# Performance work log

Measured on AMD Instinct MI355X. Metric: run time of the kernel, lower is better.

## Reference

```python
import jax, jax.numpy as jnp
import numpy as np

B, N, T, D, H = 64, 207, 24, 128, 8
DK = D // H
EPS = 1e-5


def setup_inputs() -> dict:
    key = jax.random.key(0)
    ks = jax.random.split(key, 18)
    s = 1.0 / np.sqrt(D)
    inp = {
        "hidden": jax.random.normal(ks[0], (B, N, T, D), jnp.float32),
        "matrix": jax.random.uniform(ks[1], (B, T, N, N), jnp.float32) / N,
        "Wq": jax.random.normal(ks[2], (D, D), jnp.float32) * s,
        "bq": jnp.zeros((D,), jnp.float32),
        "Wk": jax.random.normal(ks[3], (D, D), jnp.float32) * s,
        "bk": jnp.zeros((D,), jnp.float32),
        "Wv": jax.random.normal(ks[4], (D, D), jnp.float32) * s,
        "bv": jnp.zeros((D,), jnp.float32),
        "Wo": jax.random.normal(ks[5], (D, D), jnp.float32) * s,
        "bo": jnp.zeros((D,), jnp.float32),
        "Wgcn": jax.random.normal(ks[6], (D, D), jnp.float32) * s,
        "bgcn": jnp.zeros((D,), jnp.float32),
        "Wgate": jax.random.normal(ks[7], (D, 2 * D), jnp.float32) * (1.0 / np.sqrt(2 * D)),
        "bgate": jnp.zeros((D,), jnp.float32),
        "gamma": jnp.ones((D,), jnp.float32),
        "beta": jnp.zeros((D,), jnp.float32),
    }
    return inp


def reference(hidden, matrix, Wq, bq, Wk, bk, Wv, bv, Wo, bo,
              Wgcn, bgcn, Wgate, bgate, gamma, beta):
    # ---- GCN branch: per-timestep A·X then channel mixing (dmodel->dmodel)
    # hidden: [B,N,T,D], matrix: [B,T,N,N] -> aggregated [B,N,T,D]
    agg = jnp.einsum('bntc,btnm->bmtc', hidden, matrix)
    gcn_out = agg @ Wgcn.T + bgcn                       # [B,N,T,D]

    # ---- Causal multi-head temporal attention
    q = (hidden @ Wq.T + bq).reshape(B, N, T, H, DK)
    k = (hidden @ Wk.T + bk).reshape(B, N, T, H, DK)
    v = (hidden @ Wv.T + bv).reshape(B, N, T, H, DK)
    scale = 1.0 / np.sqrt(DK)
    scores = jnp.einsum('bnthe,bnshe->bnhts', q, k)     # [B,N,H,T,T]
    causal = jnp.triu(jnp.ones((T, T), bool), k=1)      # mask future
    scores = jnp.where(causal, -jnp.inf, scores)
    attn = jax.nn.softmax(scale * scores, axis=-1)
    ctx = jnp.einsum('bnhts,bnshd->bnthd', attn, v).reshape(B, N, T, D)
    attn_out = ctx @ Wo.T + bo                          # [B,N,T,D]

    # ---- Gated fusion: concat -> linear -> batchnorm (training stats) -> sigmoid
    gate_in = jnp.concatenate([gcn_out, attn_out], axis=-1)  # [B,N,T,2D]
    g = gate_in @ Wgate.T + bgate                            # [B,N,T,D]
    mean = jnp.mean(g, axis=(0, 1, 2))
    var = jnp.var(g, axis=(0, 1, 2))
    g = (g - mean) * jax.lax.rsqrt(var + EPS) * gamma + beta
    z = jax.nn.sigmoid(g)
    return z * gcn_out + (1.0 - z) * attn_out
```

## Files before the change

kernel.cpp:

```cpp
#include <hip/hip_runtime.h>

#define B_ 64
#define N_ 207
#define T_ 24
#define D_ 128
#define H_ 8
#define MROWS (B_*N_*T_)
#define SELEMS ((size_t)MROWS * D_)
#define NBLK_FB 768
#define BNROWS_FB 414
#define NBLK_FUSED (MROWS/128)
#define EPS_ 1e-5f

typedef __attribute__((ext_vector_type(8))) short s16x8;
typedef __attribute__((ext_vector_type(4))) float f32x4;

#define MFMA16(a,b,c) __builtin_amdgcn_mfma_f32_16x16x32_bf16(a,b,c,0,0,0)

__device__ __forceinline__ float bfu2f(unsigned short u) {
  return __uint_as_float(((unsigned int)u) << 16);
}
__device__ __forceinline__ unsigned short f2bfu(float f) {
  unsigned int x = __float_as_uint(f);
  return (unsigned short)((x + 0x7fffu + ((x >> 16) & 1u)) >> 16);
}
__device__ __forceinline__ unsigned int packbf2(float lo, float hi) {
  return (unsigned int)f2bfu(lo) | ((unsigned int)f2bfu(hi) << 16);
}

__global__ __launch_bounds__(256) void k_wcast(
    const float* __restrict__ Wq, const float* __restrict__ Wk,
    const float* __restrict__ Wv, const float* __restrict__ Wo,
    const float* __restrict__ Wgcn, const float* __restrict__ Wgate,
    unsigned short* __restrict__ out)
{
  const int idx4 = (blockIdx.x * 256 + threadIdx.x) * 4;
  if (idx4 >= 114688) return;
  const float* src; int off;
  if      (idx4 < 16384) { src = Wq;    off = idx4; }
  else if (idx4 < 32768) { src = Wk;    off = idx4 - 16384; }
  else if (idx4 < 49152) { src = Wv;    off = idx4 - 32768; }
  else if (idx4 < 65536) { src = Wo;    off = idx4 - 49152; }
  else if (idx4 < 81920) { src = Wgcn;  off = idx4 - 65536; }
  else                   { src = Wgate; off = idx4 - 81920; }
  const float4 v = *(const float4*)(src + off);
  ushort4 u;
  u.x = f2bfu(v.x); u.y = f2bfu(v.y); u.z = f2bfu(v.z); u.w = f2bfu(v.w);
  *(ushort4*)(out + idx4) = u;
}

__device__ __forceinline__ void gcn_load(
    const float* __restrict__ mbase, const float* __restrict__ hbase,
    int m0, int nn, int cb, int ch,
    float va[8], float vb[8], float ha[8], float hb[8])
{
  const int n_r0 = ch*32 + nn, n_r1 = n_r0 + 1;
  const bool rv0 = (n_r0 < N_), rv1 = (n_r1 < N_);
  const size_t nc0 = (size_t)(rv0 ? n_r0 : 0);
  const size_t nc1 = (size_t)(rv1 ? n_r1 : 0);
  {
    const float* r0 = mbase + nc0*N_ + m0 + cb;
    const float* r1 = mbase + nc1*N_ + m0 + cb;
    #pragma unroll
    for (int j = 0; j < 2; ++j) {
      const int mg = m0 + cb + j*4;
      if (mg + 3 < N_) {
        const float4 x0 = *(const float4*)(r0 + j*4);
        const float4 x1 = *(const float4*)(r1 + j*4);
        va[j*4+0]=x0.x; va[j*4+1]=x0.y; va[j*4+2]=x0.z; va[j*4+3]=x0.w;
        vb[j*4+0]=x1.x; vb[j*4+1]=x1.y; vb[j*4+2]=x1.z; vb[j*4+3]=x1.w;
      } else {
        #pragma unroll
        for (int e = 0; e < 4; ++e) {
          const bool ok = (mg + e) < N_;
          va[j*4+e] = ok ? r0[j*4+e] : 0.f;
          vb[j*4+e] = ok ? r1[j*4+e] : 0.f;
        }
      }
    }
    #pragma unroll
    for (int e = 0; e < 8; ++e) {
      if (!rv0) va[e] = 0.f;
      if (!rv1) vb[e] = 0.f;
    }
  }
  {
    const float* r0 = hbase + nc0*(T_*D_) + cb;
    const float* r1 = hbase + nc1*(T_*D_) + cb;
    const float4 x0a = *(const float4*)(r0);
    const float4 x0b = *(const float4*)(r0 + 4);
    const float4 x1a = *(const float4*)(r1);
    const float4 x1b = *(const float4*)(r1 + 4);
    ha[0]=x0a.x; ha[1]=x0a.y; ha[2]=x0a.z; ha[3]=x0a.w;
    ha[4]=x0b.x; ha[5]=x0b.y; ha[6]=x0b.z; ha[7]=x0b.w;
    hb[0]=x1a.x; hb[1]=x1a.y; hb[2]=x1a.z; hb[3]=x1a.w;
    hb[4]=x1b.x; hb[5]=x1b.y; hb[6]=x1b.z; hb[7]=x1b.w;
    #pragma unroll
    for (int e = 0; e < 8; ++e) {
      if (!rv0) ha[e] = 0.f;
      if (!rv1) hb[e] = 0.f;
    }
  }
}

__global__ __launch_bounds__(256) void k_gcn2(
    const float* __restrict__ hidden, const float* __restrict__ matrix,
    const unsigned short* __restrict__ Wgcnb, const float* __restrict__ bgcn,
    unsigned short* __restrict__ gcn)
{
  __shared__ __align__(16) unsigned char smem[40960];
  unsigned short* GsAll = (unsigned short*)smem;

  const int tid = threadIdx.x;
  const int w = tid >> 6, l = tid & 63;
  const int lr = l & 15, lg = l >> 4;
  const int m0 = blockIdx.x * 128;
  const int by = (int)blockIdx.y;
  const int b = by / T_, t = by % T_;

  const int nn = (tid & 15) * 2;
  const int cb = (tid >> 4) * 8;

  const float* mbase = matrix + (size_t)(b*T_ + t)*N_*N_;
  const float* hbase = hidden + (size_t)b*N_*T_*D_ + (size_t)t*D_;

  f32x4 acc1[2][8];
  #pragma unroll
  for (int mt = 0; mt < 2; mt++)
    #pragma unroll
    for (int nt = 0; nt < 8; nt++)
      #pragma unroll
      for (int e = 0; e < 4; e++) acc1[mt][nt][e] = 0.f;

  float va[8], vb[8], ha[8], hb[8];
  gcn_load(mbase, hbase, m0, nn, cb, 0, va, vb, ha, hb);

  #pragma unroll
  for (int ch = 0; ch < 7; ++ch) {
    unsigned char* base = smem + ((ch & 1) ? 20480 : 0);
    unsigned int* M32 = (unsigned int*)base;
    unsigned int* H32 = (unsigned int*)(base + 10240);
    #pragma unroll
    for (int e = 0; e < 8; ++e)
      M32[(cb + e)*20 + (tid & 15)] = packbf2(va[e], vb[e]);
    #pragma unroll
    for (int e = 0; e < 8; ++e)
      H32[(cb + e)*20 + (tid & 15)] = packbf2(ha[e], hb[e]);
    if (ch < 6)
      gcn_load(mbase, hbase, m0, nn, cb, ch + 1, va, vb, ha, hb);
    __syncthreads();
    const unsigned short* M16 = (const unsigned short*)M32;
    const unsigned short* H16 = (const unsigned short*)H32;
    const s16x8 af0 = *(const s16x8*)(M16 + (size_t)(w*32 +  0 + lr)*40 + lg*8);
    const s16x8 af1 = *(const s16x8*)(M16 + (size_t)(w*32 + 16 + lr)*40 + lg*8);
    #pragma unroll
    for (int nt = 0; nt < 8; ++nt) {
      const s16x8 bf = *(const s16x8*)(H16 + (size_t)(nt*16 + lr)*40 + lg*8);
      acc1[0][nt] = MFMA16(af0, bf, acc1[0][nt]);
      acc1[1][nt] = MFMA16(af1, bf, acc1[1][nt]);
    }
  }

  __syncthreads();
  unsigned short* gs = GsAll + (size_t)w * (32*136);
  #pragma unroll
  for (int nt = 0; nt < 8; nt++)
    #pragma unroll
    for (int mt = 0; mt < 2; mt++)
      #pragma unroll
      for (int r = 0; r < 4; r++)
        gs[(mt*16 + lg*4 + r)*136 + nt*16 + lr] = f2bfu(acc1[mt][nt][r]);

  f32x4 acc2[2][8];
  #pragma unroll
  for (int mt = 0; mt < 2; mt++)
    #pragma unroll
    for (int nt = 0; nt < 8; nt++)
      #pragma unroll
      for (int e = 0; e < 4; e++) acc2[mt][nt][e] = 0.f;

  #pragma unroll
  for (int ks = 0; ks < 4; ++ks) {
    const s16x8 a0 = *(const s16x8*)(gs + (size_t)( 0 + lr)*136 + ks*32 + lg*8);
    const s16x8 a1 = *(const s16x8*)(gs + (size_t)(16 + lr)*136 + ks*32 + lg*8);
    #pragma unroll
    for (int nt = 0; nt < 8; ++nt) {
      const s16x8 bf = *(const s16x8*)(Wgcnb + (size_t)(nt*16 + lr)*D_ + ks*32 + lg*8);
      acc2[0][nt] = MFMA16(a0, bf, acc2[0][nt]);
      acc2[1][nt] = MFMA16(a1, bf, acc2[1][nt]);
    }
  }

  #pragma unroll
  for (int nt = 0; nt < 8; nt++) {
    const float bsc = bgcn[nt*16 + lr];
    #pragma unroll
    for (int mt = 0; mt < 2; mt++)
      #pragma unroll
      for (int r = 0; r < 4; r++)
        gs[(mt*16 + lg*4 + r)*136 + nt*16 + lr] = f2bfu(acc2[mt][nt][r] + bsc);
  }
  const size_t Obase = ((size_t)b*N_ + (m0 + w*32))*(size_t)(T_*D_) + (size_t)t*D_;
  #pragma unroll
  for (int p = 0; p < 8; p++) {
    const int c = p*64 + l;
    const int row = c >> 4, c8 = (c & 15) * 8;
    const int gm = m0 + w*32 + row;
    if (gm < N_) {
      const s16x8 v = *(const s16x8*)(gs + row*136 + c8);
      *(s16x8*)(gcn + Obase + (size_t)row*(T_*D_) + c8) = v;
    }
  }
}

__global__ __launch_bounds__(256) void k_attn3(
    const float* __restrict__ hidden,
    const unsigned short* __restrict__ Wqb, const unsigned short* __restrict__ Wkb,
    const unsigned short* __restrict__ Wvb, const unsigned short* __restrict__ Wob,
    const float* __restrict__ bq, const float* __restrict__ bk,
    const float* __restrict__ bv, const float* __restrict__ bo,
    unsigned short* __restrict__ attnO)
{
  __shared__ __align__(16) unsigned short Xs[32*136];
  __shared__ __align__(16) unsigned short Qs[32*136];
  __shared__ __align__(16) unsigned short Ks[32*136];
  __shared__ __align__(16) unsigned short Vt[128*40];
  __shared__ __align__(16) unsigned short Ps[4][32*40];
  const int tid = threadIdx.x;
  const int w = tid >> 6, l = tid & 63;
  const int lr = l & 15, lg = l >> 4;
  const size_t bn = blockIdx.x;
  const float* X = hidden + bn * (size_t)(T_*D_);

  for (int i = tid; i < 32*16; i += 256) {
    const int row = i >> 4, g8 = (i & 15) * 8;
    s16x8 v;
    if (row < T_) {
      const float4 a  = *(const float4*)(X + (size_t)row*D_ + g8);
      const float4 b2 = *(const float4*)(X + (size_t)row*D_ + g8 + 4);
      v[0]=(short)f2bfu(a.x);  v[1]=(short)f2bfu(a.y);
      v[2]=(short)f2bfu(a.z);  v[3]=(short)f2bfu(a.w);
      v[4]=(short)f2bfu(b2.x); v[5]=(short)f2bfu(b2.y);
      v[6]=(short)f2bfu(b2.z); v[7]=(short)f2bfu(b2.w);
    } else {
      #pragma unroll
      for (int e = 0; e < 8; e++) v[e] = 0;
    }
    *(s16x8*)&Xs[row*136 + g8] = v;
  }
  __syncthreads();

  s16x8 af[2][4];
  #pragma unroll
  for (int mt = 0; mt < 2; mt++)
    #pragma unroll
    for (int ks = 0; ks < 4; ks++)
      af[mt][ks] = *(const s16x8*)&Xs[(mt*16 + lr)*136 + ks*32 + lg*8];
  __syncthreads();

  const unsigned short* Wp[3] = {Wqb, Wkb, Wvb};
  const float*          bp[3] = {bq, bk, bv};
  #pragma unroll
  for (int o = 0; o < 3; o++) {
    f32x4 acc[2][2];
    #pragma unroll
    for (int mt = 0; mt < 2; mt++)
      #pragma unroll
      for (int nt = 0; nt < 2; nt++)
        #pragma unroll
        for (int e = 0; e < 4; e++) acc[mt][nt][e] = 0.f;
    #pragma unroll
    for (int ks = 0; ks < 4; ks++) {
      #pragma unroll
      for (int nt = 0; nt < 2; nt++) {
        const s16x8 bf = *(const s16x8*)(Wp[o] + (size_t)(w*32 + nt*16 + lr)*D_ + ks*32 + lg*8);
        acc[0][nt] = MFMA16(af[0][ks], bf, acc[0][nt]);
        acc[1][nt] = MFMA16(af[1][ks], bf, acc[1][nt]);
      }
    }
    #pragma unroll
    for (int nt = 0; nt < 2; nt++) {
      const float bb = bp[o][w*32 + nt*16 + lr];
      #pragma unroll
      for (int mt = 0; mt < 2; mt++)
        #pragma unroll
        for (int r = 0; r < 4; r++) {
          const unsigned short hv = f2bfu(acc[mt][nt][r] + bb);
          const int trow = mt*16 + lg*4 + r;
          const int dcol = w*32 + nt*16 + lr;
          if (o == 0)      Qs[trow*136 + dcol] = hv;
          else if (o == 1) Ks[trow*136 + dcol] = hv;
          else             Vt[dcol*40 + trow] = hv;
        }
    }
  }

  unsigned short* Pw = Ps[w];
  #pragma unroll
  for (int hi = 0; hi < 2; hi++) {
    const int hh = 2*w + hi;
    s16x8 zv;
    #pragma unroll
    for (int e = 0; e < 8; e++) zv[e] = 0;
    s16x8 aq[2], bkf[2];
    #pragma unroll
    for (int mt = 0; mt < 2; mt++) {
      s16x8 tv = zv;
      if (lg < 2) tv = *(const s16x8*)&Qs[(mt*16 + lr)*136 + hh*16 + lg*8];
      aq[mt] = tv;
    }
    #pragma unroll
    for (int nt = 0; nt < 2; nt++) {
      s16x8 tv = zv;
      if (lg < 2) tv = *(const s16x8*)&Ks[(nt*16 + lr)*136 + hh*16 + lg*8];
      bkf[nt] = tv;
    }
    f32x4 accS[2][2];
    #pragma unroll
    for (int mt = 0; mt < 2; mt++)
      #pragma unroll
      for (int nt = 0; nt < 2; nt++) {
        f32x4 z4; z4[0]=0.f; z4[1]=0.f; z4[2]=0.f; z4[3]=0.f;
        accS[mt][nt] = MFMA16(aq[mt], bkf[nt], z4);
      }
    #pragma unroll
    for (int mt = 0; mt < 2; mt++) {
      #pragma unroll
      for (int r = 0; r < 4; r++) {
        const int t = mt*16 + lg*4 + r;
        const bool m0 = (lr <= t), m1 = (16 + lr <= t);
        float e0 = m0 ? __expf(0.25f * accS[mt][0][r]) : 0.f;
        float e1 = m1 ? __expf(0.25f * accS[mt][1][r]) : 0.f;
        float den = e0 + e1;
        den += __shfl_xor(den, 1);
        den += __shfl_xor(den, 2);
        den += __shfl_xor(den, 4);
        den += __shfl_xor(den, 8);
        const float rd = 1.f / den;
        Pw[t*40 + lr]      = f2bfu(e0 * rd);
        Pw[t*40 + 16 + lr] = f2bfu(e1 * rd);
      }
    }
    s16x8 ap[2];
    #pragma unroll
    for (int mt = 0; mt < 2; mt++)
      ap[mt] = *(const s16x8*)&Pw[(mt*16 + lr)*40 + lg*8];
    const s16x8 bvf = *(const s16x8*)&Vt[(hh*16 + lr)*40 + lg*8];
    f32x4 accP[2];
    #pragma unroll
    for (int mt = 0; mt < 2; mt++) {
      f32x4 z4; z4[0]=0.f; z4[1]=0.f; z4[2]=0.f; z4[3]=0.f;
      accP[mt] = MFMA16(ap[mt], bvf, z4);
    }
    #pragma unroll
    for (int mt = 0; mt < 2; mt++)
      #pragma unroll
      for (int r = 0; r < 4; r++) {
        const int t = mt*16 + lg*4 + r;
        if (t < T_) Xs[t*136 + hh*16 + lr] = f2bfu(accP[mt][r]);
      }
  }
  __syncthreads();

  s16x8 cf[2][4];
  #pragma unroll
  for (int mt = 0; mt < 2; mt++)
    #pragma unroll
    for (int ks = 0; ks < 4; ks++)
      cf[mt][ks] = *(const s16x8*)&Xs[(mt*16 + lr)*136 + ks*32 + lg*8];
  f32x4 acc2[2][2];
  #pragma unroll
  for (int mt = 0; mt < 2; mt++)
    #pragma unroll
    for (int nt = 0; nt < 2; nt++)
      #pragma unroll
      for (int e = 0; e < 4; e++) acc2[mt][nt][e] = 0.f;
  #pragma unroll
  for (int ks = 0; ks < 4; ks++) {
    #pragma unroll
    for (int nt = 0; nt < 2; nt++) {
      const s16x8 bf = *(const s16x8*)(Wob + (size_t)(w*32 + nt*16 + lr)*D_ + ks*32 + lg*8);
      acc2[0][nt] = MFMA16(cf[0][ks], bf, acc2[0][nt]);
      acc2[1][nt] = MFMA16(cf[1][ks], bf, acc2[1][nt]);
    }
  }
  #pragma unroll
  for (int nt = 0; nt < 2; nt++) {
    const float bb = bo[w*32 + nt*16 + lr];
    #pragma unroll
    for (int mt = 0; mt < 2; mt++)
      #pragma unroll
      for (int r = 0; r < 4; r++)
        Qs[(mt*16 + lg*4 + r)*136 + w*32 + nt*16 + lr] =
            f2bfu(acc2[mt][nt][r] + bb);
  }
  __syncthreads();
  unsigned short* O = attnO + bn * (size_t)(T_*D_);
  for (int i = tid; i < 24*16; i += 256) {
    const int row = i >> 4, g8 = (i & 15) * 8;
    *(s16x8*)(O + (size_t)row*D_ + g8) = *(const s16x8*)&Qs[row*136 + g8];
  }
}

template<bool STATS>
__global__ __launch_bounds__(256) void k_gate(
    const unsigned short* __restrict__ A0, const unsigned short* __restrict__ A1,
    const unsigned short* __restrict__ Wb, const float* __restrict__ bias,
    float* __restrict__ Out, float* __restrict__ psum, float* __restrict__ psq)
{
  __shared__ float lbs[4*128], lbq[4*128];
  const int tid = threadIdx.x;
  const int w = tid >> 6, l = tid & 63;
  const int lr = l & 15, lg = l >> 4;
  const size_t m0 = (size_t)blockIdx.x * 128 + w * 32;

  f32x4 acc[2][8];
  #pragma unroll
  for (int mt = 0; mt < 2; mt++)
    #pragma unroll
    for (int nt = 0; nt < 8; nt++)
      #pragma unroll
      for (int e = 0; e < 4; e++) acc[mt][nt][e] = 0.f;

  #pragma unroll
  for (int ks = 0; ks < 8; ks++) {
    const unsigned short* Asrc = (ks >= 4) ? A1 : A0;
    const int kk = (ks >= 4) ? ks - 4 : ks;
    const s16x8 a0 = *(const s16x8*)(Asrc + (m0 +  0 + lr)*D_ + kk*32 + lg*8);
    const s16x8 a1 = *(const s16x8*)(Asrc + (m0 + 16 + lr)*D_ + kk*32 + lg*8);
    #pragma unroll
    for (int nt = 0; nt < 8; nt++) {
      const s16x8 bf = *(const s16x8*)(Wb + (size_t)(nt*16 + lr)*256 + ks*32 + lg*8);
      acc[0][nt] = MFMA16(a0, bf, acc[0][nt]);
      acc[1][nt] = MFMA16(a1, bf, acc[1][nt]);
    }
  }

  #pragma unroll
  for (int nt = 0; nt < 8; nt++) {
    const float b = bias[nt*16 + lr];
    float s = 0.f, q = 0.f;
    #pragma unroll
    for (int mt = 0; mt < 2; mt++)
      #pragma unroll
      for (int r = 0; r < 4; r++) {
        const float v = acc[mt][nt][r] + b;
        Out[(m0 + mt*16 + lg*4 + r)*D_ + nt*16 + lr] = v;
        if (STATS) { s += v; q += v*v; }
      }
    if (STATS) {
      s += __shfl_xor(s, 16); s += __shfl_xor(s, 32);
      q += __shfl_xor(q, 16); q += __shfl_xor(q, 32);
      if (lg == 0) {
        lbs[w*128 + nt*16 + lr] = s;
        lbq[w*128 + nt*16 + lr] = q;
      }
    }
  }
  if (STATS) {
    __syncthreads();
    if (tid < 128) {
      const float ss = lbs[tid] + lbs[128 + tid] + lbs[256 + tid] + lbs[384 + tid];
      const float qq = lbq[tid] + lbq[128 + tid] + lbq[256 + tid] + lbq[384 + tid];
      psum[(size_t)blockIdx.x*128 + tid] = ss;
      psq [(size_t)blockIdx.x*128 + tid] = qq;
    }
  }
}

__global__ __launch_bounds__(256) void k_bnstats(
    const float* __restrict__ g, float* __restrict__ psum, float* __restrict__ psq)
{
  const int tid = threadIdx.x;
  const int c4 = (tid & 31) * 4, sub = tid >> 5;
  const size_t r0 = (size_t)blockIdx.x * BNROWS_FB;
  float4 s = make_float4(0.f,0.f,0.f,0.f), q = make_float4(0.f,0.f,0.f,0.f);
  for (int i = sub; i < BNROWS_FB; i += 8) {
    const float4 x = *(const float4*)(g + (r0 + i)*D_ + c4);
    s.x += x.x; s.y += x.y; s.z += x.z; s.w += x.w;
    q.x += x.x*x.x; q.y += x.y*x.y; q.z += x.z*x.z; q.w += x.w*x.w;
  }
  __shared__ float ls[8*128], lq[8*128];
  *(float4*)&ls[sub*128 + c4] = s;
  *(float4*)&lq[sub*128 + c4] = q;
  __syncthreads();
  if (tid < 128) {
    float ss = 0.f, qq = 0.f;
    #pragma unroll
    for (int k = 0; k < 8; k++) { ss += ls[k*128 + tid]; qq += lq[k*128 + tid]; }
    psum[(size_t)blockIdx.x*128 + tid] = ss;
    psq [(size_t)blockIdx.x*128 + tid] = qq;
  }
}

__global__ __launch_bounds__(1024) void k_bnfinal(
    const float* __restrict__ psum, const float* __restrict__ psq, int nblk,
    float* __restrict__ meanv, float* __restrict__ invstdv)
{
  const int tid = threadIdx.x;
  const int sub = tid >> 7, ch = tid & 127;
  float s = 0.f, q = 0.f;
  for (int i = sub; i < nblk; i += 8) {
    s += psum[(size_t)i*128 + ch];
    q += psq [(size_t)i*128 + ch];
  }
  __shared__ float ls[8*128], lq[8*128];
  ls[sub*128 + ch] = s; lq[sub*128 + ch] = q;
  __syncthreads();
  if (tid < 128) {
    float ss = 0.f, qq = 0.f;
    #pragma unroll
    for (int k = 0; k < 8; k++) { ss += ls[k*128 + tid]; qq += lq[k*128 + tid]; }
    const float mean = ss / (float)MROWS;
    const float var  = qq / (float)MROWS - mean*mean;
    meanv[tid] = mean;
    invstdv[tid] = rsqrtf(var + EPS_);
  }
}

__global__ __launch_bounds__(256) void k_final(
    float* __restrict__ g,
    const unsigned short* __restrict__ gcn, const unsigned short* __restrict__ attn,
    const float* __restrict__ meanv, const float* __restrict__ invstdv,
    const float* __restrict__ gamma, const float* __restrict__ beta)
{
  const size_t tot4 = SELEMS >> 2;
  for (size_t i4 = (size_t)blockIdx.x*blockDim.x + threadIdx.x; i4 < tot4;
       i4 += (size_t)gridDim.x*blockDim.x) {
    const int c4 = (int)(i4 & 31) * 4;
    const float4 gv = ((const float4*)g)[i4];
    const ushort4 gc = ((const ushort4*)gcn)[i4];
    const ushort4 at = ((const ushort4*)attn)[i4];
    const float4 m4 = *(const float4*)(meanv + c4);
    const float4 s4 = *(const float4*)(invstdv + c4);
    const float4 ga = *(const float4*)(gamma + c4);
    const float4 be = *(const float4*)(beta + c4);
    float4 outv;
    { const float y = (gv.x - m4.x)*s4.x*ga.x + be.x;
      const float z = 1.f/(1.f + __expf(-y));
      outv.x = z*bfu2f(gc.x) + (1.f - z)*bfu2f(at.x); }
    { const float y = (gv.y - m4.y)*s4.y*ga.y + be.y;
      const float z = 1.f/(1.f + __expf(-y));
      outv.y = z*bfu2f(gc.y) + (1.f - z)*bfu2f(at.y); }
    { const float y = (gv.z - m4.z)*s4.z*ga.z + be.z;
      const float z = 1.f/(1.f + __expf(-y));
      outv.z = z*bfu2f(gc.z) + (1.f - z)*bfu2f(at.z); }
    { const float y = (gv.w - m4.w)*s4.w*ga.w + be.w;
      const float z = 1.f/(1.f + __expf(-y));
      outv.w = z*bfu2f(gc.w) + (1.f - z)*bfu2f(at.w); }
    ((float4*)g)[i4] = outv;
  }
}

extern "C" void kernel_launch(void* const* d_in, const int* in_sizes, int n_in,
                              void* d_out, int out_size, void* d_ws, size_t ws_size,
                              hipStream_t stream)
{
  (void)in_sizes; (void)n_in; (void)out_size;
  const float* hidden = (const float*)d_in[0];
  const float* matrix = (const float*)d_in[1];
  const float* Wq   = (const float*)d_in[2];  const float* bq    = (const float*)d_in[3];
  const float* Wk   = (const float*)d_in[4];  const float* bk    = (const float*)d_in[5];
  const float* Wv   = (const float*)d_in[6];  const float* bv    = (const float*)d_in[7];
  const float* Wo   = (const float*)d_in[8];  const float* bo    = (const float*)d_in[9];
  const float* Wgcn = (const float*)d_in[10]; const float* bgcn  = (const float*)d_in[11];
  const float* Wgate= (const float*)d_in[12]; const float* bgate = (const float*)d_in[13];
  const float* gamma= (const float*)d_in[14]; const float* beta  = (const float*)d_in[15];
  float* out = (float*)d_out;

  unsigned short* WB = (unsigned short*)d_ws;
  unsigned short* Wqb    = WB;
  unsigned short* Wkb    = WB + 16384;
  unsigned short* Wvb    = WB + 32768;
  unsigned short* Wob    = WB + 49152;
  unsigned short* Wgcnb  = WB + 65536;
  unsigned short* Wgateb = WB + 81920;
  unsigned short* X1     = WB + 114688;
  unsigned short* X2     = X1 + SELEMS;
  float* psum    = (float*)(X2 + SELEMS);

  const size_t base_bytes = (size_t)(WB + 114688 - (unsigned short*)d_ws)*2
                          + 2*SELEMS*2;
  const size_t fused_bytes = base_bytes + ((size_t)NBLK_FUSED*128*2 + 256)*4;
  const bool fused = (ws_size >= fused_bytes);
  const int nblk = fused ? NBLK_FUSED : NBLK_FB;
  float* psq     = psum + (size_t)nblk*128;
  float* meanv   = psq  + (size_t)nblk*128;
  float* invstdv = meanv + 128;

  k_wcast<<<112, 256, 0, stream>>>(Wq, Wk, Wv, Wo, Wgcn, Wgate, WB);
  k_gcn2 <<<dim3(2, B_*T_), 256, 0, stream>>>(hidden, matrix, Wgcnb, bgcn, X2);
  k_attn3<<<B_*N_, 256, 0, stream>>>(hidden, Wqb, Wkb, Wvb, Wob,
                                     bq, bk, bv, bo, X1);
  if (fused) {
    k_gate<true><<<MROWS/128, 256, 0, stream>>>(X2, X1, Wgateb, bgate, out, psum, psq);
  } else {
    k_gate<false><<<MROWS/128, 256, 0, stream>>>(X2, X1, Wgateb, bgate, out, psum, psq);
    k_bnstats<<<NBLK_FB, 256, 0, stream>>>(out, psum, psq);
  }
  k_bnfinal<<<1, 1024, 0, stream>>>(psum, psq, nblk, meanv, invstdv);
  k_final<<<2048, 256, 0, stream>>>(out, X2, X1, meanv, invstdv, gamma, beta);
}
```

Measured before the change: 750.9 us.

## Recompute gate GEMM in final pass instead of storing fp32 gate tensor

```diff
diff --git a/kernel.cpp b/kernel.cpp
--- a/kernel.cpp
+++ b/kernel.cpp
@@ -1,4 +1,5 @@
 #include <hip/hip_runtime.h>
+#include <hip/hip_bf16.h>
 
 #define B_ 64
 #define N_ 207
@@ -21,8 +22,9 @@
   return __uint_as_float(((unsigned int)u) << 16);
 }
 __device__ __forceinline__ unsigned short f2bfu(float f) {
-  unsigned int x = __float_as_uint(f);
-  return (unsigned short)((x + 0x7fffu + ((x >> 16) & 1u)) >> 16);
+  union { __hip_bfloat16 h; unsigned short u; } cv;
+  cv.h = __float2bfloat16(f);
+  return cv.u;
 }
 __device__ __forceinline__ unsigned int packbf2(float lo, float hi) {
   return (unsigned int)f2bfu(lo) | ((unsigned int)f2bfu(hi) << 16);
@@ -234,19 +236,16 @@
 
   for (int i = tid; i < 32*16; i += 256) {
     const int row = i >> 4, g8 = (i & 15) * 8;
-    s16x8 v;
     if (row < T_) {
       const float4 a  = *(const float4*)(X + (size_t)row*D_ + g8);
       const float4 b2 = *(const float4*)(X + (size_t)row*D_ + g8 + 4);
-      v[0]=(short)f2bfu(a.x);  v[1]=(short)f2bfu(a.y);
-      v[2]=(short)f2bfu(a.z);  v[3]=(short)f2bfu(a.w);
-      v[4]=(short)f2bfu(b2.x); v[5]=(short)f2bfu(b2.y);
-      v[6]=(short)f2bfu(b2.z); v[7]=(short)f2bfu(b2.w);
+      uint4 u;
+      u.x = packbf2(a.x, a.y);   u.y = packbf2(a.z, a.w);
+      u.z = packbf2(b2.x, b2.y); u.w = packbf2(b2.z, b2.w);
+      *(uint4*)&Xs[row*136 + g8] = u;
     } else {
-      #pragma unroll
-      for (int e = 0; e < 8; e++) v[e] = 0;
-    }
-    *(s16x8*)&Xs[row*136 + g8] = v;
+      *(uint4*)&Xs[row*136 + g8] = make_uint4(0,0,0,0);
+    }
   }
   __syncthreads();
 
@@ -296,12 +295,12 @@
   }
 
   unsigned short* Pw = Ps[w];
+  s16x8 zv;
+  #pragma unroll
+  for (int e = 0; e < 8; e++) zv[e] = 0;
   #pragma unroll
   for (int hi = 0; hi < 2; hi++) {
     const int hh = 2*w + hi;
-    s16x8 zv;
-    #pragma unroll
-    for (int e = 0; e < 8; e++) zv[e] = 0;
     s16x8 aq[2], bkf[2];
     #pragma unroll
     for (int mt = 0; mt < 2; mt++) {
@@ -402,7 +401,7 @@
   }
 }
 
-template<bool STATS>
+template<bool WRITEG, bool STATS>
 __global__ __launch_bounds__(256) void k_gate(
     const unsigned short* __restrict__ A0, const unsigned short* __restrict__ A1,
     const unsigned short* __restrict__ Wb, const float* __restrict__ bias,
@@ -445,7 +444,7 @@
       #pragma unroll
       for (int r = 0; r < 4; r++) {
         const float v = acc[mt][nt][r] + b;
-        Out[(m0 + mt*16 + lg*4 + r)*D_ + nt*16 + lr] = v;
+        if (WRITEG) Out[(m0 + mt*16 + lg*4 + r)*D_ + nt*16 + lr] = v;
         if (STATS) { s += v; q += v*v; }
       }
     if (STATS) {
@@ -468,6 +467,77 @@
   }
 }
 
+__global__ __launch_bounds__(256) void k_final2(
+    const unsigned short* __restrict__ A0, const unsigned short* __restrict__ A1,
+    const unsigned short* __restrict__ Wb, const float* __restrict__ bias,
+    const float* __restrict__ scalev, const float* __restrict__ shiftv,
+    float* __restrict__ Out)
+{
+  __shared__ __align__(16) unsigned short lb[4][32*136];
+  const int tid = threadIdx.x;
+  const int w = tid >> 6, l = tid & 63;
+  const int lr = l & 15, lg = l >> 4;
+  const size_t m0 = (size_t)blockIdx.x * 128 + w * 32;
+
+  f32x4 acc[2][8];
+  #pragma unroll
+  for (int mt = 0; mt < 2; mt++)
+    #pragma unroll
+    for (int nt = 0; nt < 8; nt++)
+      #pragma unroll
+      for (int e = 0; e < 4; e++) acc[mt][nt][e] = 0.f;
+
+  #pragma unroll
+  for (int ks = 0; ks < 8; ks++) {
+    const unsigned short* Asrc = (ks >= 4) ? A1 : A0;
+    const int kk = (ks >= 4) ? ks - 4 : ks;
+    const s16x8 a0 = *(const s16x8*)(Asrc + (m0 +  0 + lr)*D_ + kk*32 + lg*8);
+    const s16x8 a1 = *(const s16x8*)(Asrc + (m0 + 16 + lr)*D_ + kk*32 + lg*8);
+    #pragma unroll
+    for (int nt = 0; nt < 8; nt++) {
+      const s16x8 bf = *(const s16x8*)(Wb + (size_t)(nt*16 + lr)*256 + ks*32 + lg*8);
+      acc[0][nt] = MFMA16(a0, bf, acc[0][nt]);
+      acc[1][nt] = MFMA16(a1, bf, acc[1][nt]);
+    }
+  }
+
+  #pragma unroll
+  for (int nt = 0; nt < 8; nt++) {
+    const float b = bias[nt*16 + lr];
+    #pragma unroll
+    for (int mt = 0; mt < 2; mt++)
+      #pragma unroll
+      for (int r = 0; r < 4; r++)
+        lb[w][(mt*16 + lg*4 + r)*136 + nt*16 + lr] = f2bfu(acc[mt][nt][r] + b);
+  }
+  #pragma unroll
+  for (int p = 0; p < 8; p++) {
+    const int c = p*64 + l;
+    const int row = c >> 4, c8 = (c & 15) * 8;
+    const size_t grow = m0 + row;
+    const s16x8 g8  = *(const s16x8*)&lb[w][row*136 + c8];
+    const s16x8 gc8 = *(const s16x8*)(A0 + grow*D_ + c8);
+    const s16x8 at8 = *(const s16x8*)(A1 + grow*D_ + c8);
+    const float4 sc0 = *(const float4*)(scalev + c8);
+    const float4 sc1 = *(const float4*)(scalev + c8 + 4);
+    const float4 sh0 = *(const float4*)(shiftv + c8);
+    const float4 sh1 = *(const float4*)(shiftv + c8 + 4);
+    const float scv[8] = {sc0.x,sc0.y,sc0.z,sc0.w,sc1.x,sc1.y,sc1.z,sc1.w};
+    const float shv[8] = {sh0.x,sh0.y,sh0.z,sh0.w,sh1.x,sh1.y,sh1.z,sh1.w};
+    float o[8];
+    #pragma unroll
+    for (int e = 0; e < 8; e++) {
+      const float y = bfu2f((unsigned short)g8[e]) * scv[e] + shv[e];
+      const float z = 1.f / (1.f + __expf(-y));
+      o[e] = z * bfu2f((unsigned short)gc8[e])
+           + (1.f - z) * bfu2f((unsigned short)at8[e]);
+    }
+    float* orow = Out + grow*D_ + c8;
+    *(float4*)orow       = make_float4(o[0], o[1], o[2], o[3]);
+    *(float4*)(orow + 4) = make_float4(o[4], o[5], o[6], o[7]);
+  }
+}
+
 __global__ __launch_bounds__(256) void k_bnstats(
     const float* __restrict__ g, float* __restrict__ psum, float* __restrict__ psq)
 {
@@ -495,7 +565,8 @@
 
 __global__ __launch_bounds__(1024) void k_bnfinal(
     const float* __restrict__ psum, const float* __restrict__ psq, int nblk,
-    float* __restrict__ meanv, float* __restrict__ invstdv)
+    const float* __restrict__ gamma, const float* __restrict__ beta,
+    float* __restrict__ scalev, float* __restrict__ shiftv)
 {
   const int tid = threadIdx.x;
   const int sub = tid >> 7, ch = tid & 127;
@@ -513,16 +584,17 @@
     for (int k = 0; k < 8; k++) { ss += ls[k*128 + tid]; qq += lq[k*128 + tid]; }
     const float mean = ss / (float)MROWS;
     const float var  = qq / (float)MROWS - mean*mean;
-    meanv[tid] = mean;
-    invstdv[tid] = rsqrtf(var + EPS_);
+    const float istd = rsqrtf(var + EPS_);
+    const float sc = istd * gamma[tid];
+    scalev[tid] = sc;
+    shiftv[tid] = beta[tid] - mean * sc;
   }
 }
 
 __global__ __launch_bounds__(256) void k_final(
     float* __restrict__ g,
     const unsigned short* __restrict__ gcn, const unsigned short* __restrict__ attn,
-    const float* __restrict__ meanv, const float* __restrict__ invstdv,
-    const float* __restrict__ gamma, const float* __restrict__ beta)
+    const float* __restrict__ scalev, const float* __restrict__ shiftv)
 {
   const size_t tot4 = SELEMS >> 2;
   for (size_t i4 = (size_t)blockIdx.x*blockDim.x + threadIdx.x; i4 < tot4;
@@ -531,21 +603,19 @@
     const float4 gv = ((const float4*)g)[i4];
     const ushort4 gc = ((const ushort4*)gcn)[i4];
     const ushort4 at = ((const ushort4*)attn)[i4];
-    const float4 m4 = *(const float4*)(meanv + c4);
-    const float4 s4 = *(const float4*)(invstdv + c4);
-    const float4 ga = *(const float4*)(gamma + c4);
-    const float4 be = *(const float4*)(beta + c4);
+    const float4 sc = *(const float4*)(scalev + c4);
+    const float4 sh = *(const float4*)(shiftv + c4);
     float4 outv;
-    { const float y = (gv.x - m4.x)*s4.x*ga.x + be.x;
+    { const float y = gv.x*sc.x + sh.x;
       const float z = 1.f/(1.f + __expf(-y));
       outv.x = z*bfu2f(gc.x) + (1.f - z)*bfu2f(at.x); }
-    { const float y = (gv.y - m4.y)*s4.y*ga.y + be.y;
+    { const float y = gv.y*sc.y + sh.y;
       const float z = 1.f/(1.f + __expf(-y));
       outv.y = z*bfu2f(gc.y) + (1.f - z)*bfu2f(at.y); }
-    { const float y = (gv.z - m4.z)*s4.z*ga.z + be.z;
+    { const float y = gv.z*sc.z + sh.z;
       const float z = 1.f/(1.f + __expf(-y));
       outv.z = z*bfu2f(gc.z) + (1.f - z)*bfu2f(at.z); }
-    { const float y = (gv.w - m4.w)*s4.w*ga.w + be.w;
+    { const float y = gv.w*sc.w + sh.w;
       const float z = 1.f/(1.f + __expf(-y));
       outv.w = z*bfu2f(gc.w) + (1.f - z)*bfu2f(at.w); }
     ((float4*)g)[i4] = outv;
@@ -585,19 +655,24 @@
   const bool fused = (ws_size >= fused_bytes);
   const int nblk = fused ? NBLK_FUSED : NBLK_FB;
   float* psq     = psum + (size_t)nblk*128;
-  float* meanv   = psq  + (size_t)nblk*128;
-  float* invstdv = meanv + 128;
+  float* scalev  = psq  + (size_t)nblk*128;
+  float* shiftv  = scalev + 128;
 
   k_wcast<<<112, 256, 0, stream>>>(Wq, Wk, Wv, Wo, Wgcn, Wgate, WB);
   k_gcn2 <<<dim3(2, B_*T_), 256, 0, stream>>>(hidden, matrix, Wgcnb, bgcn, X2);
   k_attn3<<<B_*N_, 256, 0, stream>>>(hidden, Wqb, Wkb, Wvb, Wob,
                                      bq, bk, bv, bo, X1);
   if (fused) {
-    k_gate<true><<<MROWS/128, 256, 0, stream>>>(X2, X1, Wgateb, bgate, out, psum, psq);
+    k_gate<false,true><<<MROWS/128, 256, 0, stream>>>(X2, X1, Wgateb, bgate,
+                                                      out, psum, psq);
+    k_bnfinal<<<1, 1024, 0, stream>>>(psum, psq, nblk, gamma, beta, scalev, shiftv);
+    k_final2<<<MROWS/128, 256, 0, stream>>>(X2, X1, Wgateb, bgate,
+                                            scalev, shiftv, out);
   } else {
-    k_gate<false><<<MROWS/128, 256, 0, stream>>>(X2, X1, Wgateb, bgate, out, psum, psq);
+    k_gate<true,false><<<MROWS/128, 256, 0, stream>>>(X2, X1, Wgateb, bgate,
+                                                      out, psum, psq);
     k_bnstats<<<NBLK_FB, 256, 0, stream>>>(out, psum, psq);
-  }
-  k_bnfinal<<<1, 1024, 0, stream>>>(psum, psq, nblk, meanv, invstdv);
-  k_final<<<2048, 256, 0, stream>>>(out, X2, X1, meanv, invstdv, gamma, beta);
-}
+    k_bnfinal<<<1, 1024, 0, stream>>>(psum, psq, nblk, gamma, beta, scalev, shiftv);
+    k_final<<<2048, 256, 0, stream>>>(out, X2, X1, scalev, shiftv);
+  }
+}
```

New measurement: 755.1 us. No clear change (+0.6%).
